# Kernel optimization log

Measured on AMD Instinct MI355X. Metric: run time of the kernel, lower is better.

Reference implementation:

```python
import jax, jax.numpy as jnp
import numpy as np

B, T, D = 4, 4096, 1024
H = D // 4  # size // size_to_hidden = 256
SIZE_TO_HIDDEN = 4


def setup_inputs() -> dict:
    key = jax.random.key(0)
    k1, k2, k3, k4 = jax.random.split(key, 4)
    return {
        "inputs": jax.random.normal(k1, (B, T, D), dtype=jnp.float32),
        "W_q": jax.random.normal(k2, (D, H), dtype=jnp.float32),
        "W_k": jax.random.normal(k3, (D, H), dtype=jnp.float32),
        "W_v": jax.random.normal(k4, (D, H), dtype=jnp.float32),
    }


def reference(inputs, W_q, W_k, W_v):
    # Q, K, V: [B, T, H]
    Q = jnp.einsum('btd,dh->bth', inputs, W_q)
    K = jnp.einsum('btd,dh->bth', inputs, W_k)
    V = jnp.einsum('btd,dh->bth', inputs, W_v)
    # logits: [B, T, T]; NOTE: original scales by sqrt(size_to_hidden), not sqrt(d_k)
    logits = jnp.einsum('bqh,bkh->bqk', Q, K) / jnp.sqrt(jnp.float32(SIZE_TO_HIDDEN))
    alpha = jax.nn.softmax(logits, axis=-1)
    return jnp.einsum('bqk,bkh->bqh', alpha, V)  # [B, T, H]
```

## Files before the change

kernel.cpp:

```cpp
#include <hip/hip_runtime.h>
#include <hip/hip_fp16.h>
#include <math.h>

#define TDIM 4096
#define DDIM 1024
#define HDIM 256
#define BB   4

typedef _Float16 f16;
typedef f16  half8  __attribute__((ext_vector_type(8)));
typedef float floatx4 __attribute__((ext_vector_type(4)));

union U4 { uint4 u; half8 h; };

#define KPITCH 264
#define VPITCH 40

__device__ inline unsigned pk16(float a, float b) {
  auto r = __builtin_amdgcn_cvt_pkrtz(a, b);
  return __builtin_bit_cast(unsigned, r);
}

__global__ __launch_bounds__(256) void qkv_gemm(
    const float* __restrict__ A,
    const float* __restrict__ Wq, const float* __restrict__ Wk, const float* __restrict__ Wv,
    float* __restrict__ Qs, f16* __restrict__ Khi, f16* __restrict__ Klo,
    f16* __restrict__ Vt)
{
  __shared__ float sAt[16][68];
  __shared__ float sB[16][68];
  const int tid = threadIdx.x;
  const int tx = tid & 15, ty = tid >> 4;
  const int m0 = blockIdx.x * 64;
  const int nt = blockIdx.y;
  const int w  = nt >> 2;
  const int n0 = (nt & 3) * 64;
  const float* W = (w == 0) ? Wq : (w == 1) ? Wk : Wv;

  const int ar = tid >> 2, ac = (tid & 3) * 4;
  const int br = tid >> 4, bc = (tid & 15) * 4;

  float acc[4][4] = {};
  for (int k0 = 0; k0 < DDIM; k0 += 16) {
    float4 av = *reinterpret_cast<const float4*>(&A[(size_t)(m0 + ar) * DDIM + k0 + ac]);
    float4 bv = *reinterpret_cast<const float4*>(&W[(size_t)(k0 + br) * HDIM + n0 + bc]);
    __syncthreads();
    sAt[ac + 0][ar] = av.x; sAt[ac + 1][ar] = av.y;
    sAt[ac + 2][ar] = av.z; sAt[ac + 3][ar] = av.w;
    *reinterpret_cast<float4*>(&sB[br][bc]) = bv;
    __syncthreads();
#pragma unroll
    for (int kk = 0; kk < 16; ++kk) {
      float4 a4 = *reinterpret_cast<const float4*>(&sAt[kk][4 * ty]);
      float4 b4 = *reinterpret_cast<const float4*>(&sB[kk][4 * tx]);
      float a_[4] = {a4.x, a4.y, a4.z, a4.w};
      float b_[4] = {b4.x, b4.y, b4.z, b4.w};
#pragma unroll
      for (int i = 0; i < 4; ++i)
#pragma unroll
        for (int j = 0; j < 4; ++j)
          acc[i][j] = fmaf(a_[i], b_[j], acc[i][j]);
    }
  }
#pragma unroll
  for (int i = 0; i < 4; ++i) {
    const int mrow = m0 + 4 * ty + i;
    if (w == 0) {
      float4 o4 = {acc[i][0] * 0.5f, acc[i][1] * 0.5f, acc[i][2] * 0.5f, acc[i][3] * 0.5f};
      *reinterpret_cast<float4*>(&Qs[(size_t)mrow * HDIM + n0 + 4 * tx]) = o4;
    } else if (w == 1) {
#pragma unroll
      for (int j = 0; j < 4; ++j) {
        float x = acc[i][j];
        f16 hi = (f16)x;
        Khi[(size_t)mrow * HDIM + n0 + 4 * tx + j] = hi;
        Klo[(size_t)mrow * HDIM + n0 + 4 * tx + j] = (f16)(x - (float)hi);
      }
    } else {
      const int bb = mrow >> 12, t = mrow & 4095;
#pragma unroll
      for (int j = 0; j < 4; ++j)
        Vt[(size_t)bb * HDIM * TDIM + (size_t)(n0 + 4 * tx + j) * TDIM + t] = (f16)acc[i][j];
    }
  }
}

__global__ __launch_bounds__(256) void attn_mfma(
    const float* __restrict__ Qs, const f16* __restrict__ Khi,
    const f16* __restrict__ Klo, const f16* __restrict__ Vt,
    float* __restrict__ O)
{
  __shared__ f16 sKhi[32 * KPITCH];
  __shared__ f16 sKlo[32 * KPITCH];
  __shared__ f16 sVt[256 * VPITCH];

  const int tid = threadIdx.x;
  const int lane = tid & 63;
  const int wv = tid >> 6;
  const int ql = lane & 15;
  const int g  = lane >> 4;

  const int i = blockIdx.x;
  const int b = (i & 7) >> 1;
  const int p = ((i >> 3) << 1) | (i & 1);
  const size_t tb = (size_t)b * TDIM;

  const int q0 = p * 64 + wv * 16;

  half8 qhi[8], qlo[8];
  {
    const float* qr = Qs + (tb + q0 + ql) * HDIM;
#pragma unroll
    for (int hc = 0; hc < 8; ++hc) {
      const float* src = qr + hc * 32 + g * 8;
      half8 h, l;
#pragma unroll
      for (int j = 0; j < 8; ++j) {
        float x = src[j];
        f16 hi = (f16)x;
        h[j] = hi;
        l[j] = (f16)(x - (float)hi);
      }
      qhi[hc] = h; qlo[hc] = l;
    }
  }

  floatx4 o[16];
#pragma unroll
  for (int t = 0; t < 16; ++t) o[t] = (floatx4){0.f, 0.f, 0.f, 0.f};
  float m_run = -INFINITY, l_run = 0.f;

  const f16* gKhi = Khi + tb * HDIM;
  const f16* gKlo = Klo + tb * HDIM;
  const f16* gVt  = Vt + (size_t)b * HDIM * TDIM;

  uint4 rkh[4], rkl[4], rv[4];
#pragma unroll
  for (int s = 0; s < 4; ++s) {
    int flat = tid + 256 * s;
    int kr = flat >> 5, kc = flat & 31;
    rkh[s] = *(const uint4*)(gKhi + (size_t)kr * HDIM + kc * 8);
    rkl[s] = *(const uint4*)(gKlo + (size_t)kr * HDIM + kc * 8);
    int vh = flat >> 2, vc = flat & 3;
    rv[s] = *(const uint4*)(gVt + (size_t)vh * TDIM + vc * 8);
  }

  for (int it = 0; it < TDIM / 32; ++it) {
    __syncthreads();
#pragma unroll
    for (int s = 0; s < 4; ++s) {
      int flat = tid + 256 * s;
      int kr = flat >> 5, kc = flat & 31;
      *(uint4*)(sKhi + kr * KPITCH + kc * 8) = rkh[s];
      *(uint4*)(sKlo + kr * KPITCH + kc * 8) = rkl[s];
      int vh = flat >> 2, vc = flat & 3;
      *(uint4*)(sVt + vh * VPITCH + vc * 8) = rv[s];
    }
    __syncthreads();
    if (it + 1 < TDIM / 32) {
      const int kb = (it + 1) * 32;
#pragma unroll
      for (int s = 0; s < 4; ++s) {
        int flat = tid + 256 * s;
        int kr = flat >> 5, kc = flat & 31;
        rkh[s] = *(const uint4*)(gKhi + (size_t)(kb + kr) * HDIM + kc * 8);
        rkl[s] = *(const uint4*)(gKlo + (size_t)(kb + kr) * HDIM + kc * 8);
        int vh = flat >> 2, vc = flat & 3;
        rv[s] = *(const uint4*)(gVt + (size_t)vh * TDIM + kb + vc * 8);
      }
    }

    floatx4 st0 = {0.f, 0.f, 0.f, 0.f}, st1 = {0.f, 0.f, 0.f, 0.f};
#pragma unroll
    for (int hc = 0; hc < 8; ++hc) {
      U4 a0h, a0l, a1h, a1l;
      a0h.u = *(const uint4*)(sKhi + (0 + ql) * KPITCH + hc * 32 + g * 8);
      a0l.u = *(const uint4*)(sKlo + (0 + ql) * KPITCH + hc * 32 + g * 8);
      a1h.u = *(const uint4*)(sKhi + (16 + ql) * KPITCH + hc * 32 + g * 8);
      a1l.u = *(const uint4*)(sKlo + (16 + ql) * KPITCH + hc * 32 + g * 8);
      st0 = __builtin_amdgcn_mfma_f32_16x16x32_f16(a0h.h, qhi[hc], st0, 0, 0, 0);
      st1 = __builtin_amdgcn_mfma_f32_16x16x32_f16(a1h.h, qhi[hc], st1, 0, 0, 0);
      st0 = __builtin_amdgcn_mfma_f32_16x16x32_f16(a0h.h, qlo[hc], st0, 0, 0, 0);
      st1 = __builtin_amdgcn_mfma_f32_16x16x32_f16(a1h.h, qlo[hc], st1, 0, 0, 0);
      st0 = __builtin_amdgcn_mfma_f32_16x16x32_f16(a0l.h, qhi[hc], st0, 0, 0, 0);
      st1 = __builtin_amdgcn_mfma_f32_16x16x32_f16(a1l.h, qhi[hc], st1, 0, 0, 0);
    }

    float mx = fmaxf(fmaxf(fmaxf(st0[0], st0[1]), fmaxf(st0[2], st0[3])),
                     fmaxf(fmaxf(st1[0], st1[1]), fmaxf(st1[2], st1[3])));
    mx = fmaxf(mx, __shfl_xor(mx, 16, 64));
    mx = fmaxf(mx, __shfl_xor(mx, 32, 64));
    float alpha = 1.f;
    if (__any(mx > m_run)) {
      float mnew = fmaxf(m_run, mx);
      alpha = __expf(m_run - mnew);
      m_run = mnew;
      float a0 = __shfl(alpha, 4 * g + 0, 64);
      float a1 = __shfl(alpha, 4 * g + 1, 64);
      float a2 = __shfl(alpha, 4 * g + 2, 64);
      float a3 = __shfl(alpha, 4 * g + 3, 64);
#pragma unroll
      for (int t = 0; t < 16; ++t) {
        o[t][0] *= a0; o[t][1] *= a1; o[t][2] *= a2; o[t][3] *= a3;
      }
    }
    float pv0 = __expf(st0[0] - m_run), pv1 = __expf(st0[1] - m_run);
    float pv2 = __expf(st0[2] - m_run), pv3 = __expf(st0[3] - m_run);
    float pv4 = __expf(st1[0] - m_run), pv5 = __expf(st1[1] - m_run);
    float pv6 = __expf(st1[2] - m_run), pv7 = __expf(st1[3] - m_run);
    float sum = ((pv0 + pv1) + (pv2 + pv3)) + ((pv4 + pv5) + (pv6 + pv7));
    sum += __shfl_xor(sum, 16, 64);
    sum += __shfl_xor(sum, 32, 64);
    l_run = l_run * alpha + sum;

    unsigned P0 = pk16(pv0, pv1), P1 = pk16(pv2, pv3);
    unsigned P2 = pk16(pv4, pv5), P3 = pk16(pv6, pv7);
    const int sA = ql + ((g & 1) << 5);
    const int sB = sA + 16;
    unsigned s0A = __shfl(P0, sA, 64), s2A = __shfl(P2, sA, 64);
    unsigned s1A = __shfl(P1, sA, 64), s3A = __shfl(P3, sA, 64);
    unsigned s0B = __shfl(P0, sB, 64), s2B = __shfl(P2, sB, 64);
    unsigned s1B = __shfl(P1, sB, 64), s3B = __shfl(P3, sB, 64);
    U4 paU;
    paU.u.x = (g < 2) ? s0A : s2A;
    paU.u.y = (g < 2) ? s1A : s3A;
    paU.u.z = (g < 2) ? s0B : s2B;
    paU.u.w = (g < 2) ? s1B : s3B;

#pragma unroll
    for (int t = 0; t < 16; ++t) {
      U4 vb;
      vb.u = *(const uint4*)(sVt + (t * 16 + ql) * VPITCH + g * 8);
      o[t] = __builtin_amdgcn_mfma_f32_16x16x32_f16(paU.h, vb.h, o[t], 0, 0, 0);
    }
  }

  float r0 = 1.f / __shfl(l_run, 4 * g + 0, 64);
  float r1 = 1.f / __shfl(l_run, 4 * g + 1, 64);
  float r2 = 1.f / __shfl(l_run, 4 * g + 2, 64);
  float r3 = 1.f / __shfl(l_run, 4 * g + 3, 64);
#pragma unroll
  for (int t = 0; t < 16; ++t) {
    O[(tb + q0 + 4 * g + 0) * HDIM + t * 16 + ql] = o[t][0] * r0;
    O[(tb + q0 + 4 * g + 1) * HDIM + t * 16 + ql] = o[t][1] * r1;
    O[(tb + q0 + 4 * g + 2) * HDIM + t * 16 + ql] = o[t][2] * r2;
    O[(tb + q0 + 4 * g + 3) * HDIM + t * 16 + ql] = o[t][3] * r3;
  }
}

extern "C" void kernel_launch(void* const* d_in, const int* in_sizes, int n_in,
                              void* d_out, int out_size, void* d_ws, size_t ws_size,
                              hipStream_t stream) {
  const float* inp = (const float*)d_in[0];
  const float* Wq  = (const float*)d_in[1];
  const float* Wk  = (const float*)d_in[2];
  const float* Wv  = (const float*)d_in[3];
  float* out = (float*)d_out;

  float* Qs = (float*)d_ws;
  f16* KhiP = (f16*)((char*)d_ws + (size_t)16384 * 256 * 4);
  f16* KloP = KhiP + (size_t)16384 * 256;
  f16* VtP  = KloP + (size_t)16384 * 256;

  qkv_gemm<<<dim3(16384 / 64, 12), 256, 0, stream>>>(inp, Wq, Wk, Wv, Qs, KhiP, KloP, VtP);
  attn_mfma<<<dim3(256), 256, 0, stream>>>(Qs, KhiP, KloP, VtP, out);
}
```

Before: 955.5 us.

## Split attention over key halves with merge kernel, vectorize QKV epilogue stores

The attention kernel now splits each query block's key range into two halves. This doubles the grid from 256 to 512 blocks, which fills more of the GPU's compute units, and adds launch_bounds occupancy 2. Each half writes an unnormalized partial output plus its running max and sum, and a new merge kernel combines them, at the cost of extra workspace traffic and one more launch. Separately, the QKV GEMM epilogue packs K stores into uint2 writes and transposes V through shared memory for coalesced stores. It also vectorizes Q loads and splits the MFMA accumulators into independent chains, and the softmax max is only rescaled when it grows by more than 8.

```diff
diff --git a/kernel.cpp b/kernel.cpp
--- a/kernel.cpp
+++ b/kernel.cpp
@@ -6,12 +6,15 @@
 #define DDIM 1024
 #define HDIM 256
 #define BB   4
+#define NROWS (BB * TDIM)
+#define NIT   64
 
 typedef _Float16 f16;
 typedef f16  half8  __attribute__((ext_vector_type(8)));
 typedef float floatx4 __attribute__((ext_vector_type(4)));
 
 union U4 { uint4 u; half8 h; };
+union U2 { uint2 u; f16 h[4]; };
 
 #define KPITCH 264
 #define VPITCH 40
@@ -29,6 +32,7 @@
 {
   __shared__ float sAt[16][68];
   __shared__ float sB[16][68];
+  __shared__ f16 sT[64][72];
   const int tid = threadIdx.x;
   const int tx = tid & 15, ty = tid >> 4;
   const int m0 = blockIdx.x * 64;
@@ -62,33 +66,48 @@
           acc[i][j] = fmaf(a_[i], b_[j], acc[i][j]);
     }
   }
-#pragma unroll
-  for (int i = 0; i < 4; ++i) {
-    const int mrow = m0 + 4 * ty + i;
-    if (w == 0) {
+  if (w == 0) {
+#pragma unroll
+    for (int i = 0; i < 4; ++i) {
       float4 o4 = {acc[i][0] * 0.5f, acc[i][1] * 0.5f, acc[i][2] * 0.5f, acc[i][3] * 0.5f};
-      *reinterpret_cast<float4*>(&Qs[(size_t)mrow * HDIM + n0 + 4 * tx]) = o4;
-    } else if (w == 1) {
+      *reinterpret_cast<float4*>(&Qs[(size_t)(m0 + 4 * ty + i) * HDIM + n0 + 4 * tx]) = o4;
+    }
+  } else if (w == 1) {
+#pragma unroll
+    for (int i = 0; i < 4; ++i) {
+      U2 hh, ll;
 #pragma unroll
       for (int j = 0; j < 4; ++j) {
         float x = acc[i][j];
         f16 hi = (f16)x;
-        Khi[(size_t)mrow * HDIM + n0 + 4 * tx + j] = hi;
-        Klo[(size_t)mrow * HDIM + n0 + 4 * tx + j] = (f16)(x - (float)hi);
+        hh.h[j] = hi;
+        ll.h[j] = (f16)(x - (float)hi);
       }
-    } else {
-      const int bb = mrow >> 12, t = mrow & 4095;
+      size_t off = (size_t)(m0 + 4 * ty + i) * HDIM + n0 + 4 * tx;
+      *reinterpret_cast<uint2*>(&Khi[off]) = hh.u;
+      *reinterpret_cast<uint2*>(&Klo[off]) = ll.u;
+    }
+  } else {
+#pragma unroll
+    for (int i = 0; i < 4; ++i)
 #pragma unroll
       for (int j = 0; j < 4; ++j)
-        Vt[(size_t)bb * HDIM * TDIM + (size_t)(n0 + 4 * tx + j) * TDIM + t] = (f16)acc[i][j];
-    }
-  }
-}
-
-__global__ __launch_bounds__(256) void attn_mfma(
+        sT[4 * tx + j][4 * ty + i] = (f16)acc[i][j];
+    __syncthreads();
+    const int row = tid >> 2, seg = tid & 3;
+    uint4 w0 = *reinterpret_cast<uint4*>(&sT[row][seg * 16]);
+    uint4 w1 = *reinterpret_cast<uint4*>(&sT[row][seg * 16 + 8]);
+    size_t gb = (size_t)(m0 >> 12) * HDIM * TDIM + (size_t)(n0 + row) * TDIM
+              + (m0 & 4095) + seg * 16;
+    *reinterpret_cast<uint4*>(&Vt[gb]) = w0;
+    *reinterpret_cast<uint4*>(&Vt[gb + 8]) = w1;
+  }
+}
+
+__global__ __launch_bounds__(256, 2) void attn_mfma(
     const float* __restrict__ Qs, const f16* __restrict__ Khi,
     const f16* __restrict__ Klo, const f16* __restrict__ Vt,
-    float* __restrict__ O)
+    float* __restrict__ Po, float* __restrict__ Pm, float* __restrict__ Pl)
 {
   __shared__ f16 sKhi[32 * KPITCH];
   __shared__ f16 sKlo[32 * KPITCH];
@@ -101,10 +120,12 @@
   const int g  = lane >> 4;
 
   const int i = blockIdx.x;
-  const int b = (i & 7) >> 1;
-  const int p = ((i >> 3) << 1) | (i & 1);
+  const int sel = i & 7;
+  const int b = sel >> 1;
+  const int half = sel & 1;
+  const int p = i >> 3;
   const size_t tb = (size_t)b * TDIM;
-
+  const int koff = half * 2048;
   const int q0 = p * 64 + wv * 16;
 
   half8 qhi[8], qlo[8];
@@ -113,13 +134,15 @@
 #pragma unroll
     for (int hc = 0; hc < 8; ++hc) {
       const float* src = qr + hc * 32 + g * 8;
+      float4 u0 = *reinterpret_cast<const float4*>(src);
+      float4 u1 = *reinterpret_cast<const float4*>(src + 4);
+      float xs[8] = {u0.x, u0.y, u0.z, u0.w, u1.x, u1.y, u1.z, u1.w};
       half8 h, l;
 #pragma unroll
       for (int j = 0; j < 8; ++j) {
-        float x = src[j];
-        f16 hi = (f16)x;
+        f16 hi = (f16)xs[j];
         h[j] = hi;
-        l[j] = (f16)(x - (float)hi);
+        l[j] = (f16)(xs[j] - (float)hi);
       }
       qhi[hc] = h; qlo[hc] = l;
     }
@@ -139,13 +162,13 @@
   for (int s = 0; s < 4; ++s) {
     int flat = tid + 256 * s;
     int kr = flat >> 5, kc = flat & 31;
-    rkh[s] = *(const uint4*)(gKhi + (size_t)kr * HDIM + kc * 8);
-    rkl[s] = *(const uint4*)(gKlo + (size_t)kr * HDIM + kc * 8);
+    rkh[s] = *(const uint4*)(gKhi + (size_t)(koff + kr) * HDIM + kc * 8);
+    rkl[s] = *(const uint4*)(gKlo + (size_t)(koff + kr) * HDIM + kc * 8);
     int vh = flat >> 2, vc = flat & 3;
-    rv[s] = *(const uint4*)(gVt + (size_t)vh * TDIM + vc * 8);
-  }
-
-  for (int it = 0; it < TDIM / 32; ++it) {
+    rv[s] = *(const uint4*)(gVt + (size_t)vh * TDIM + koff + vc * 8);
+  }
+
+  for (int it = 0; it < NIT; ++it) {
     __syncthreads();
 #pragma unroll
     for (int s = 0; s < 4; ++s) {
@@ -157,8 +180,8 @@
       *(uint4*)(sVt + vh * VPITCH + vc * 8) = rv[s];
     }
     __syncthreads();
-    if (it + 1 < TDIM / 32) {
-      const int kb = (it + 1) * 32;
+    if (it + 1 < NIT) {
+      const int kb = koff + (it + 1) * 32;
 #pragma unroll
       for (int s = 0; s < 4; ++s) {
         int flat = tid + 256 * s;
@@ -170,7 +193,8 @@
       }
     }
 
-    floatx4 st0 = {0.f, 0.f, 0.f, 0.f}, st1 = {0.f, 0.f, 0.f, 0.f};
+    floatx4 c0 = {0,0,0,0}, c1 = {0,0,0,0}, c2 = {0,0,0,0};
+    floatx4 c3 = {0,0,0,0}, c4 = {0,0,0,0}, c5 = {0,0,0,0};
 #pragma unroll
     for (int hc = 0; hc < 8; ++hc) {
       U4 a0h, a0l, a1h, a1l;
@@ -178,20 +202,22 @@
       a0l.u = *(const uint4*)(sKlo + (0 + ql) * KPITCH + hc * 32 + g * 8);
       a1h.u = *(const uint4*)(sKhi + (16 + ql) * KPITCH + hc * 32 + g * 8);
       a1l.u = *(const uint4*)(sKlo + (16 + ql) * KPITCH + hc * 32 + g * 8);
-      st0 = __builtin_amdgcn_mfma_f32_16x16x32_f16(a0h.h, qhi[hc], st0, 0, 0, 0);
-      st1 = __builtin_amdgcn_mfma_f32_16x16x32_f16(a1h.h, qhi[hc], st1, 0, 0, 0);
-      st0 = __builtin_amdgcn_mfma_f32_16x16x32_f16(a0h.h, qlo[hc], st0, 0, 0, 0);
-      st1 = __builtin_amdgcn_mfma_f32_16x16x32_f16(a1h.h, qlo[hc], st1, 0, 0, 0);
-      st0 = __builtin_amdgcn_mfma_f32_16x16x32_f16(a0l.h, qhi[hc], st0, 0, 0, 0);
-      st1 = __builtin_amdgcn_mfma_f32_16x16x32_f16(a1l.h, qhi[hc], st1, 0, 0, 0);
-    }
+      c0 = __builtin_amdgcn_mfma_f32_16x16x32_f16(a0h.h, qhi[hc], c0, 0, 0, 0);
+      c3 = __builtin_amdgcn_mfma_f32_16x16x32_f16(a1h.h, qhi[hc], c3, 0, 0, 0);
+      c1 = __builtin_amdgcn_mfma_f32_16x16x32_f16(a0h.h, qlo[hc], c1, 0, 0, 0);
+      c4 = __builtin_amdgcn_mfma_f32_16x16x32_f16(a1h.h, qlo[hc], c4, 0, 0, 0);
+      c2 = __builtin_amdgcn_mfma_f32_16x16x32_f16(a0l.h, qhi[hc], c2, 0, 0, 0);
+      c5 = __builtin_amdgcn_mfma_f32_16x16x32_f16(a1l.h, qhi[hc], c5, 0, 0, 0);
+    }
+    floatx4 st0 = (c0 + c1) + c2;
+    floatx4 st1 = (c3 + c4) + c5;
 
     float mx = fmaxf(fmaxf(fmaxf(st0[0], st0[1]), fmaxf(st0[2], st0[3])),
                      fmaxf(fmaxf(st1[0], st1[1]), fmaxf(st1[2], st1[3])));
     mx = fmaxf(mx, __shfl_xor(mx, 16, 64));
     mx = fmaxf(mx, __shfl_xor(mx, 32, 64));
     float alpha = 1.f;
-    if (__any(mx > m_run)) {
+    if (__any(mx > m_run + 8.f)) {
       float mnew = fmaxf(m_run, mx);
       alpha = __expf(m_run - mnew);
       m_run = mnew;
@@ -235,16 +261,38 @@
     }
   }
 
-  float r0 = 1.f / __shfl(l_run, 4 * g + 0, 64);
-  float r1 = 1.f / __shfl(l_run, 4 * g + 1, 64);
-  float r2 = 1.f / __shfl(l_run, 4 * g + 2, 64);
-  float r3 = 1.f / __shfl(l_run, 4 * g + 3, 64);
+  float* Pob = Po + (size_t)half * NROWS * HDIM;
 #pragma unroll
   for (int t = 0; t < 16; ++t) {
-    O[(tb + q0 + 4 * g + 0) * HDIM + t * 16 + ql] = o[t][0] * r0;
-    O[(tb + q0 + 4 * g + 1) * HDIM + t * 16 + ql] = o[t][1] * r1;
-    O[(tb + q0 + 4 * g + 2) * HDIM + t * 16 + ql] = o[t][2] * r2;
-    O[(tb + q0 + 4 * g + 3) * HDIM + t * 16 + ql] = o[t][3] * r3;
+    Pob[(tb + q0 + 4 * g + 0) * HDIM + t * 16 + ql] = o[t][0];
+    Pob[(tb + q0 + 4 * g + 1) * HDIM + t * 16 + ql] = o[t][1];
+    Pob[(tb + q0 + 4 * g + 2) * HDIM + t * 16 + ql] = o[t][2];
+    Pob[(tb + q0 + 4 * g + 3) * HDIM + t * 16 + ql] = o[t][3];
+  }
+  if (g == 0) {
+    Pm[(size_t)half * NROWS + tb + q0 + ql] = m_run;
+    Pl[(size_t)half * NROWS + tb + q0 + ql] = l_run;
+  }
+}
+
+__global__ __launch_bounds__(256) void attn_merge(
+    const float* __restrict__ Po, const float* __restrict__ Pm,
+    const float* __restrict__ Pl, float* __restrict__ O)
+{
+  const int NV4 = NROWS * HDIM / 4;
+  const float4* Po4 = (const float4*)Po;
+  float4* O4 = (float4*)O;
+  for (int e = blockIdx.x * 256 + threadIdx.x; e < NV4; e += 2048 * 256) {
+    int r = e >> 6;
+    float m0 = Pm[r], m1 = Pm[NROWS + r];
+    float l0 = Pl[r], l1 = Pl[NROWS + r];
+    float M = fmaxf(m0, m1);
+    float w0 = __expf(m0 - M), w1 = __expf(m1 - M);
+    float L = 1.f / (l0 * w0 + l1 * w1);
+    float4 a = Po4[e], c = Po4[NV4 + e];
+    float4 r4 = {(a.x * w0 + c.x * w1) * L, (a.y * w0 + c.y * w1) * L,
+                 (a.z * w0 + c.z * w1) * L, (a.w * w0 + c.w * w1) * L};
+    O4[e] = r4;
   }
 }
 
@@ -257,11 +305,16 @@
   const float* Wv  = (const float*)d_in[3];
   float* out = (float*)d_out;
 
-  float* Qs = (float*)d_ws;
-  f16* KhiP = (f16*)((char*)d_ws + (size_t)16384 * 256 * 4);
-  f16* KloP = KhiP + (size_t)16384 * 256;
-  f16* VtP  = KloP + (size_t)16384 * 256;
-
-  qkv_gemm<<<dim3(16384 / 64, 12), 256, 0, stream>>>(inp, Wq, Wk, Wv, Qs, KhiP, KloP, VtP);
-  attn_mfma<<<dim3(256), 256, 0, stream>>>(Qs, KhiP, KloP, VtP, out);
-}
+  char* wp = (char*)d_ws;
+  float* Qs = (float*)wp;                      wp += (size_t)NROWS * HDIM * 4;
+  f16* KhiP = (f16*)wp;                        wp += (size_t)NROWS * HDIM * 2;
+  f16* KloP = (f16*)wp;                        wp += (size_t)NROWS * HDIM * 2;
+  f16* VtP  = (f16*)wp;                        wp += (size_t)NROWS * HDIM * 2;
+  float* Po = (float*)wp;                      wp += (size_t)2 * NROWS * HDIM * 4;
+  float* Pm = (float*)wp;                      wp += (size_t)2 * NROWS * 4;
+  float* Pl = (float*)wp;
+
+  qkv_gemm<<<dim3(NROWS / 64, 12), 256, 0, stream>>>(inp, Wq, Wk, Wv, Qs, KhiP, KloP, VtP);
+  attn_mfma<<<dim3(512), 256, 0, stream>>>(Qs, KhiP, KloP, VtP, Po, Pm, Pl);
+  attn_merge<<<dim3(2048), 256, 0, stream>>>(Po, Pm, Pl, out);
+}
```

Measured after the change: 928.6 us. -2.8%, faster.
